# Performance work log

Measured on AMD Instinct MI355X. Metric: run time of the kernel, lower is better.

Reference implementation:

```python
import jax, jax.numpy as jnp
import numpy as np

B, F, V, DW, H, K, T = 32, 2048, 12000, 300, 512, 3, 32
START_ID, END_ID = 1, 2
NEG = -1e9


def lstm(x, h, c, Wx, Wh, b):
    # BasicLSTMCell with forget_bias=1.0
    z = x @ Wx + h @ Wh + b  # [N, 4H]
    i, f, g, o = jnp.split(z, 4, axis=-1)
    c2 = jax.nn.sigmoid(f + 1.0) * c + jax.nn.sigmoid(i) * jnp.tanh(g)
    h2 = jax.nn.sigmoid(o) * jnp.tanh(c2)
    return h2, c2


def beam_decode(E, Wx, Wh, b, Wl, bl, img):
    Bn = img.shape[0]
    img_t = jnp.repeat(img, K, axis=0)  # tile_batch: [B*K, F]
    h = jnp.zeros((Bn * K, H), img.dtype)
    c = jnp.zeros_like(h)
    beam_lp = jnp.tile(jnp.array([0.0] + [NEG] * (K - 1), img.dtype), (Bn, 1))  # [B,K]
    prev = jnp.full((Bn, K), START_ID, jnp.int32)
    finished = jnp.zeros((Bn, K), bool)
    lengths = jnp.zeros((Bn, K), jnp.int32)
    ids = jnp.zeros((Bn, K, T), jnp.int32)
    end_row = jnp.where(jnp.arange(V) == END_ID, 0.0, NEG)  # finished beams only emit END

    def step(carry, t):
        h, c, beam_lp, prev, finished, lengths, ids = carry
        x = jnp.concatenate([E[prev.reshape(-1)], img_t], axis=-1)  # [B*K, DW+F]
        h2, c2 = lstm(x, h, c, Wx, Wh, b)
        lp = jax.nn.log_softmax(h2 @ Wl + bl).reshape(Bn, K, V)
        lp = jnp.where(finished[:, :, None], end_row, lp)
        total = (beam_lp[:, :, None] + lp).reshape(Bn, K * V)
        scores, idx = jax.lax.top_k(total, K)  # [B,K]
        parent = idx // V
        word = (idx % V).astype(jnp.int32)
        g2 = lambda a: jnp.take_along_axis(a, parent, axis=1)
        g3 = lambda a: jnp.take_along_axis(a, parent[:, :, None], axis=1)
        h2 = g3(h2.reshape(Bn, K, H)).reshape(Bn * K, H)
        c2 = g3(c2.reshape(Bn, K, H)).reshape(Bn * K, H)
        ids = g3(ids).at[:, :, t].set(word)  # reorder hypotheses, append word
        fin_p = g2(finished)
        len_p = g2(lengths)
        lengths = jnp.where(fin_p, len_p, len_p + 1)
        finished = fin_p | (word == END_ID)
        return (h2, c2, scores, word, finished, lengths, ids), None

    carry, _ = jax.lax.scan(step, (h, c, beam_lp, prev, finished, lengths, ids), jnp.arange(T))
    return carry[6], carry[5]  # ids [B,K,T], lengths [B,K]


def teacher_rnn(E, Wx, Wh, b, img_t, seq_inputs, lengths):
    # dynamic_rnn semantics: zero outputs and frozen state past sequence_length
    N, L = seq_inputs.shape
    emb = E[seq_inputs]  # [N, L, DW]
    h0 = jnp.zeros((N, H), E.dtype)
    c0 = jnp.zeros_like(h0)

    def step(carry, xs):
        h, c = carry
        x_t, t = xs
        xin = jnp.concatenate([x_t, img_t], axis=-1)
        h2, c2 = lstm(xin, h, c, Wx, Wh, b)
        active = (t < lengths)[:, None]
        h = jnp.where(active, h2, h)
        c = jnp.where(active, c2, c)
        return (h, c), jnp.where(active, h2, 0.0)

    _, outs = jax.lax.scan(step, (h0, c0), (emb.transpose(1, 0, 2), jnp.arange(L)))
    return outs.transpose(1, 0, 2)  # [N, L, H]


def setup_inputs() -> dict:
    key = jax.random.key(0)
    ks = jax.random.split(key, 6)
    return {
        "mean_image_features": jax.random.normal(ks[0], (B, F), jnp.float32),
        "embeddings": jax.random.normal(ks[1], (V, DW), jnp.float32) * 0.1,
        "Wx": jax.random.normal(ks[2], (DW + F, 4 * H), jnp.float32) / np.sqrt(DW + F),
        "Wh": jax.random.normal(ks[3], (H, 4 * H), jnp.float32) / np.sqrt(H),
        "b_lstm": jnp.zeros((4 * H,), jnp.float32),
        "W_logits": jax.random.normal(ks[4], (H, V), jnp.float32) / np.sqrt(H),
        "b_logits": jnp.zeros((V,), jnp.float32),
    }


def reference(mean_image_features, embeddings, Wx, Wh, b_lstm, W_logits, b_logits):
    Bn = mean_image_features.shape[0]
    ids, lengths = beam_decode(embeddings, Wx, Wh, b_lstm, W_logits, b_logits, mean_image_features)
    seq_inputs = jnp.concatenate(
        [jnp.full((Bn, K, 1), START_ID, jnp.int32), ids], axis=2
    ).reshape(Bn * K, T + 1)
    img_t = jnp.repeat(mean_image_features, K, axis=0)
    acts = teacher_rnn(embeddings, Wx, Wh, b_lstm, img_t, seq_inputs, lengths.reshape(-1))
    logits = (acts @ W_logits + b_logits).reshape(Bn, K, T + 1, V)
    return logits, jnp.argmax(logits, axis=-1).astype(jnp.int32)
```

## Files before the change

kernel.cpp:

```cpp
#include <hip/hip_runtime.h>
#include <hip/hip_bf16.h>
#include <math.h>

#define NB   32
#define FDIM 2048
#define VV   12000
#define DWW  300
#define HH   512
#define KW   3
#define TDEC 32
#define SEQ  33
#define NK   96
#define G4   2048
#define START_ID 1
#define END_ID   2
#define NROWS 3168
#define NLB   188
#define INTMX 0x7fffffff
#define FLOORF (-3.0e38f)

typedef float f4v __attribute__((ext_vector_type(4)));
__device__ __forceinline__ void nt_store4(float* p, float4 v){
  f4v t; t.x=v.x; t.y=v.y; t.z=v.z; t.w=v.w;
  __builtin_nontemporal_store(t, (f4v*)p);
}

__device__ __forceinline__ float sigf(float x){ return 1.0f/(1.0f+expf(-x)); }

__device__ __forceinline__ unsigned short f2b(float x){
  __hip_bfloat16 b = __float2bfloat16(x);
  return *reinterpret_cast<unsigned short*>(&b);
}

__device__ __forceinline__ void ins3(float v, int i, float tv[3], int ti[3]){
  if (v > tv[0] || (v == tv[0] && i < ti[0])){
    tv[2]=tv[1]; ti[2]=ti[1]; tv[1]=tv[0]; ti[1]=ti[0]; tv[0]=v; ti[0]=i;
  } else if (v > tv[1] || (v == tv[1] && i < ti[1])){
    tv[2]=tv[1]; ti[2]=ti[1]; tv[1]=v; ti[1]=i;
  } else if (v > tv[2] || (v == tv[2] && i < ti[2])){
    tv[2]=v; ti[2]=i;
  }
}

struct SArgs {
  const float *E, *Wx, *Wh, *Wl, *blog;
  float *P, *c2, *h2s, *zp, *partA, *beam_lp, *rowamax;
  int *prev, *finished, *lengths, *parst, *rowsrc;
  void *Lst;
};

__global__ __launch_bounds__(128) void k_pimg(const float* __restrict__ img,
                                              const float* __restrict__ Wx,
                                              float* __restrict__ parts)
{
  int colb = blockIdx.x, fb = blockIdx.y, tid = threadIdx.x;
  int col = colb*128 + tid;
  int f0 = fb*128;
  __shared__ float s_img[32][128];
  for (int r=0;r<32;r++) s_img[r][tid] = img[r*FDIM + f0 + tid];
  __syncthreads();
  float acc[32];
  #pragma unroll
  for (int r=0;r<32;r++) acc[r]=0.f;
  for (int f2=0; f2<128; ++f2){
    float w = Wx[(size_t)(DWW + f0 + f2)*G4 + col];
    #pragma unroll
    for (int r=0;r<32;r++) acc[r] += w * s_img[r][f2];
  }
  #pragma unroll
  for (int r=0;r<32;r++) parts[(size_t)fb*(32*G4) + r*G4 + col] = acc[r];
}

__global__ __launch_bounds__(512) void k_prep(const float* __restrict__ parts,
    const float* __restrict__ bls, const float* __restrict__ blog,
    float* __restrict__ P, float* __restrict__ beam_lp, int* __restrict__ prev,
    int* __restrict__ finished, int* __restrict__ lengths, float* __restrict__ bamax)
{
  int bid = blockIdx.x, tid = threadIdx.x;
  int gid = bid*512 + tid;
  float s = bls[gid & (G4-1)];
  for (int fb=0; fb<16; ++fb) s += parts[(size_t)fb*(32*G4) + gid];
  P[gid] = s;
  if (bid==0 && tid<NK){
    beam_lp[tid] = (tid%KW==0)?0.f:-1e9f;
    prev[tid]=START_ID; finished[tid]=0; lengths[tid]=0;
  }
  if (bid==2){
    __shared__ float s_rf[8]; __shared__ int s_ri[8];
    float bv=FLOORF; int bi=INTMX;
    for (int i=tid;i<VV;i+=512){
      float v=blog[i];
      if (v>bv || (v==bv && i<bi)){ bv=v; bi=i; }
    }
    #pragma unroll
    for (int d=1;d<64;d<<=1){
      float ov=__shfl_xor(bv,d); int oi=__shfl_xor(bi,d);
      if (ov>bv || (ov==bv && oi<bi)){ bv=ov; bi=oi; }
    }
    if ((tid&63)==0){ s_rf[tid>>6]=bv; s_ri[tid>>6]=bi; }
    __syncthreads();
    if (tid==0){
      for (int w=1;w<8;w++)
        if (s_rf[w]>bv || (s_rf[w]==bv && s_ri[w]<bi)){ bv=s_rf[w]; bi=s_ri[w]; }
      bamax[0] = (float)bi;
    }
  }
}

__global__ __launch_bounds__(512) void k_z(SArgs a, int t)
{
  int bid = blockIdx.x, tid = threadIdx.x;
  __shared__ float smem[96*17 + 16*64];
  __shared__ int sprev[NK], spar[NK];
  if (t>0 && tid<NK){ sprev[tid]=a.prev[tid]; spar[tid]=a.parst[(t-1)*NK+tid]; }
  __syncthreads();

  int colblk = bid & 31, p = bid >> 5;
  int col0 = colblk*64;
  int ks = p*104, ke = ks+104; if (ke>812) ke=812;
  float* sA = smem;
  float* sB = smem + 96*17;
  int tx = tid&15, ty = tid>>4;
  float4 acc[3];
  #pragma unroll
  for (int r=0;r<3;r++) acc[r]=make_float4(0.f,0.f,0.f,0.f);
  for (int k0=ks;k0<ke;k0+=16){
    int bk = ke-k0; if (bk>16) bk=16;
    for (int i=tid;i<96*16;i+=512){
      int n=i>>4, kk=i&15;
      float v=0.f;
      if (kk<bk){
        int kg=k0+kk;
        if (kg<DWW){
          int w = (t==0)?START_ID:sprev[n];
          v = a.E[(size_t)w*DWW+kg];
        } else if (t>0){
          v = a.h2s[((size_t)(t-1)*NK + spar[n])*HH + (kg-DWW)];
        }
      }
      sA[n*17+kk]=v;
    }
    for (int i=tid;i<16*64;i+=512){
      int kk=i>>6, cc=i&63;
      float v=0.f;
      if (kk<bk){
        int kg=k0+kk;
        v = (kg<DWW) ? a.Wx[(size_t)kg*G4+col0+cc] : a.Wh[(size_t)(kg-DWW)*G4+col0+cc];
      }
      sB[i]=v;
    }
    __syncthreads();
    #pragma unroll
    for (int kk=0;kk<16;++kk){
      float4 b4 = *(const float4*)&sB[kk*64+tx*4];
      #pragma unroll
      for (int rr=0;rr<3;rr++){
        float av = sA[(ty+rr*32)*17+kk];
        acc[rr].x += av*b4.x; acc[rr].y += av*b4.y;
        acc[rr].z += av*b4.z; acc[rr].w += av*b4.w;
      }
    }
    __syncthreads();
  }
  float* zpp = a.zp + (size_t)p*NK*G4;
  #pragma unroll
  for (int rr=0;rr<3;rr++)
    *(float4*)&zpp[(size_t)(ty+rr*32)*G4 + col0 + tx*4] = acc[rr];
}

__global__ __launch_bounds__(512) void k_g(SArgs a, int t)
{
  int n = blockIdx.x, m = threadIdx.x;
  int bb = n/KW;
  int par = (t>0) ? a.parst[(t-1)*NK + n] : 0;
  const float* Pr = a.P + (size_t)bb*G4;
  float zi=Pr[m], zf=Pr[HH+m], zg=Pr[2*HH+m], zo=Pr[3*HH+m];
  for (int p=0;p<8;p++){
    const float* zz = a.zp + (size_t)p*NK*G4 + (size_t)n*G4;
    zi+=zz[m]; zf+=zz[HH+m]; zg+=zz[2*HH+m]; zo+=zz[3*HH+m];
  }
  float cold = (t==0) ? 0.f : a.c2[(size_t)((t-1)&1)*NK*HH + (size_t)par*HH + m];
  float c2v = sigf(zf+1.0f)*cold + sigf(zi)*tanhf(zg);
  float h2v = sigf(zo)*tanhf(c2v);
  a.c2[(size_t)(t&1)*NK*HH + (size_t)n*HH + m] = c2v;
  a.h2s[((size_t)t*NK+n)*HH + m] = h2v;
}

template<int BF>
__global__ __launch_bounds__(512) void k_l(SArgs a, int t)
{
  __shared__ float smem[96*36 + 32*64];
  const int bid = blockIdx.x, tid = threadIdx.x;
  const int col0 = bid*64;
  float* sAl = smem;
  float* sBl = smem + 96*36;
  const int tx=tid&15, ty=tid>>4;
  float4 acc[3];
  #pragma unroll
  for (int r=0;r<3;r++) acc[r]=make_float4(0.f,0.f,0.f,0.f);
  for (int k0=0;k0<HH;k0+=32){
    for (int i=tid;i<768;i+=512){
      int row=i>>3, kq=(i&7)*4;
      *(float4*)&sAl[row*36+kq] = *(const float4*)&a.h2s[((size_t)t*NK+row)*HH + k0+kq];
    }
    {
      int kk=tid>>4, c4=(tid&15)*4;
      int col=col0+c4;
      float4 v = make_float4(0.f,0.f,0.f,0.f);
      if (col < VV) v = *(const float4*)&a.Wl[(size_t)(k0+kk)*VV+col];
      *(float4*)&sBl[kk*64+c4]=v;
    }
    __syncthreads();
    #pragma unroll
    for (int kk=0;kk<32;++kk){
      float4 b4 = *(const float4*)&sBl[kk*64+tx*4];
      #pragma unroll
      for (int rr=0;rr<3;rr++){
        float av = sAl[(ty+rr*32)*36+kk];
        acc[rr].x += av*b4.x; acc[rr].y += av*b4.y;
        acc[rr].z += av*b4.z; acc[rr].w += av*b4.w;
      }
    }
    __syncthreads();
  }
  int colg = col0 + tx*4;
  bool cval = colg < VV;
  float4 bias = make_float4(0.f,0.f,0.f,0.f);
  if (cval) bias = *(const float4*)&a.blog[colg];
  #pragma unroll
  for (int rr=0;rr<3;rr++){
    int row = ty + rr*32;
    float v0,v1,v2,v3;
    if (cval){
      v0=acc[rr].x+bias.x; v1=acc[rr].y+bias.y;
      v2=acc[rr].z+bias.z; v3=acc[rr].w+bias.w;
      size_t off = (size_t)(t*NK+row)*VV + colg;
      if (BF){
        ushort4 u;
        u.x=f2b(v0); u.y=f2b(v1); u.z=f2b(v2); u.w=f2b(v3);
        *(ushort4*)((unsigned short*)a.Lst + off) = u;
      } else {
        nt_store4((float*)a.Lst + off, make_float4(v0,v1,v2,v3));
      }
    } else { v0=v1=v2=v3=-INFINITY; }
    float m = fmaxf(fmaxf(v0,v1),fmaxf(v2,v3));
    #pragma unroll
    for (int d=1;d<16;d<<=1) m = fmaxf(m,__shfl_xor(m,d));
    float tv[3]={-INFINITY,-INFINITY,-INFINITY};
    int   ti[3]={INTMX,INTMX,INTMX};
    float s=0.f;
    if (cval){
      ins3(v0,colg,tv,ti); ins3(v1,colg+1,tv,ti);
      ins3(v2,colg+2,tv,ti); ins3(v3,colg+3,tv,ti);
      s = expf(v0-m)+expf(v1-m)+expf(v2-m)+expf(v3-m);
    }
    #pragma unroll
    for (int d=1;d<16;d<<=1){
      s += __shfl_xor(s,d);
      float p0=__shfl_xor(tv[0],d),p1=__shfl_xor(tv[1],d),p2=__shfl_xor(tv[2],d);
      int q0=__shfl_xor(ti[0],d),q1=__shfl_xor(ti[1],d),q2=__shfl_xor(ti[2],d);
      ins3(p0,q0,tv,ti); ins3(p1,q1,tv,ti); ins3(p2,q2,tv,ti);
    }
    if (tx==0){
      float* rp = a.partA + ((size_t)row*NLB + bid)*8;
      *(float4*)rp = make_float4(m,s,tv[0],tv[1]);
      *((float4*)rp+1) = make_float4(tv[2],__int_as_float(ti[0]),__int_as_float(ti[1]),__int_as_float(ti[2]));
    }
  }
}

__global__ __launch_bounds__(512) void k_s(SArgs a, int t)
{
  __shared__ float s_lse[KW], s_tv3[KW*3];
  __shared__ int   s_ti3[KW*3];
  int b = blockIdx.x, tid = threadIdx.x;
  int wv = tid>>6, lane = tid&63;
  if (wv < KW){
    int n = b*KW+wv;
    float M=FLOORF, S=0.f;
    float tv[3]={FLOORF,FLOORF,FLOORF}; int ti[3]={INTMX,INTMX,INTMX};
    for (int i=lane;i<NLB;i+=64){
      const float* rp = a.partA + ((size_t)n*NLB+i)*8;
      float4 r0=*(const float4*)rp, r1=*((const float4*)rp+1);
      float nm = fmaxf(M,r0.x);
      S = S*expf(M-nm) + r0.y*expf(r0.x-nm);
      M = nm;
      ins3(r0.z,__float_as_int(r1.y),tv,ti);
      ins3(r0.w,__float_as_int(r1.z),tv,ti);
      ins3(r1.x,__float_as_int(r1.w),tv,ti);
    }
    #pragma unroll
    for (int d=1;d<64;d<<=1){
      float Mo=__shfl_xor(M,d), So=__shfl_xor(S,d);
      float nm=fmaxf(M,Mo);
      S = S*expf(M-nm)+So*expf(Mo-nm);
      M=nm;
      float p0=__shfl_xor(tv[0],d),p1=__shfl_xor(tv[1],d),p2=__shfl_xor(tv[2],d);
      int q0=__shfl_xor(ti[0],d),q1=__shfl_xor(ti[1],d),q2=__shfl_xor(ti[2],d);
      ins3(p0,q0,tv,ti); ins3(p1,q1,tv,ti); ins3(p2,q2,tv,ti);
    }
    if (lane==0){
      s_lse[wv] = M + logf(S);
      #pragma unroll
      for (int j=0;j<3;j++){ s_tv3[wv*3+j]=tv[j]; s_ti3[wv*3+j]=ti[j]; }
      a.rowamax[t*NK+n] = (float)ti[0];
    }
  }
  __syncthreads();
  if (tid==0){
    float cv[3]={FLOORF,FLOORF,FLOORF}; int cf[3]={INTMX,INTMX,INTMX};
    for (int k=0;k<KW;k++){
      int n=b*KW+k;
      if (a.finished[n]){
        ins3(a.beam_lp[n], k*VV+END_ID, cv,cf);
      } else {
        float blp=a.beam_lp[n], lse=s_lse[k];
        for (int j=0;j<3;j++)
          ins3(blp + (s_tv3[k*3+j]-lse), k*VV+s_ti3[k*3+j], cv,cf);
      }
    }
    int fin_old[KW], len_old[KW];
    for (int j=0;j<KW;j++){ fin_old[j]=a.finished[b*KW+j]; len_old[j]=a.lengths[b*KW+j]; }
    for (int kp=0;kp<KW;kp++){
      int par=cf[kp]/VV, word=cf[kp]-par*VV;
      a.beam_lp[b*KW+kp]=cv[kp];
      a.prev[b*KW+kp]=word;
      a.parst[t*NK + b*KW+kp] = b*KW+par;
      int fp=fin_old[par];
      a.lengths[b*KW+kp] = fp?len_old[par]:(len_old[par]+1);
      a.finished[b*KW+kp] = fp | (word==END_ID);
    }
  }
}

__global__ __launch_bounds__(128) void k_backtrack(const int* __restrict__ parst,
                                                   const int* __restrict__ lengths,
                                                   int* __restrict__ rowsrc)
{
  int n = threadIdx.x;
  if (n >= NK) return;
  int b = n / KW;
  int len = lengths[n];
  rowsrc[n*SEQ + TDEC] = -1;
  int a = n;
  for (int tau = TDEC-1; tau >= 1; --tau){
    int p = parst[tau*NK + a];
    rowsrc[n*SEQ + tau] = (tau < len) ? (tau*NK + p) : -1;
    a = p;
  }
  rowsrc[n*SEQ + 0] = b*KW;
}

template<int BF>
__global__ __launch_bounds__(512) void k_gather(const void* __restrict__ Lst,
    const int* __restrict__ rowsrc, const float* __restrict__ rowamax,
    const float* __restrict__ bamax, const float* __restrict__ blog,
    float* __restrict__ out)
{
  int row = blockIdx.x, tid = threadIdx.x;
  int src = rowsrc[row];
  float* orow = out + (size_t)row*VV;
  if (src >= 0){
    if (BF){
      const unsigned short* L = (const unsigned short*)Lst + (size_t)src*VV;
      for (int j=tid;j<VV/4;j+=512){
        ushort4 u = *(const ushort4*)&L[j*4];
        float4 v;
        v.x = __uint_as_float(((unsigned)u.x)<<16);
        v.y = __uint_as_float(((unsigned)u.y)<<16);
        v.z = __uint_as_float(((unsigned)u.z)<<16);
        v.w = __uint_as_float(((unsigned)u.w)<<16);
        nt_store4(&orow[j*4], v);
      }
    } else {
      const float* L = (const float*)Lst + (size_t)src*VV;
      for (int j=tid;j<VV/4;j+=512){
        float4 v = *(const float4*)&L[j*4];
        nt_store4(&orow[j*4], v);
      }
    }
    if (tid==0) out[(size_t)NROWS*VV + row] = rowamax[src];
  } else {
    for (int j=tid;j<VV/4;j+=512){
      float4 v = *(const float4*)&blog[j*4];
      nt_store4(&orow[j*4], v);
    }
    if (tid==0) out[(size_t)NROWS*VV + row] = bamax[0];
  }
}

extern "C" void kernel_launch(void* const* d_in, const int* in_sizes, int n_in,
                              void* d_out, int out_size, void* d_ws, size_t ws_size,
                              hipStream_t stream) {
  (void)in_sizes; (void)n_in; (void)out_size;
  const float* img  = (const float*)d_in[0];
  const float* E    = (const float*)d_in[1];
  const float* Wx   = (const float*)d_in[2];
  const float* Wh   = (const float*)d_in[3];
  const float* bls  = (const float*)d_in[4];
  const float* Wl   = (const float*)d_in[5];
  const float* blog = (const float*)d_in[6];
  float* out = (float*)d_out;

  float* ws = (float*)d_ws;
  size_t o = 0;
  float* P       = ws+o; o += (size_t)NB*G4;
  float* c2      = ws+o; o += (size_t)2*NK*HH;
  float* h2s     = ws+o; o += (size_t)TDEC*NK*HH;
  float* zp      = ws+o; o += (size_t)8*NK*G4;
  float* partA   = ws+o; o += (size_t)NK*NLB*8;
  float* beam_lp = ws+o; o += 128;
  float* rowamax = ws+o; o += (size_t)TDEC*NK;
  float* bamax   = ws+o; o += 4;
  int* prev      = (int*)(ws+o); o += 128;
  int* finished  = (int*)(ws+o); o += 128;
  int* lengths   = (int*)(ws+o); o += 128;
  int* parst     = (int*)(ws+o); o += (size_t)TDEC*NK;
  int* rowsrc    = (int*)(ws+o); o += 3328;
  o = (o+3) & ~(size_t)3;
  void* Lst      = (void*)(ws+o);

  bool f32 = (ws_size/4 > o) && ((ws_size/4 - o) >= (size_t)TDEC*NK*VV);

  SArgs a;
  a.E=E; a.Wx=Wx; a.Wh=Wh; a.Wl=Wl; a.blog=blog;
  a.P=P; a.c2=c2; a.h2s=h2s; a.zp=zp; a.partA=partA;
  a.beam_lp=beam_lp; a.rowamax=rowamax;
  a.prev=prev; a.finished=finished; a.lengths=lengths; a.parst=parst; a.rowsrc=rowsrc;
  a.Lst=Lst;

  k_pimg<<<dim3(16,16),128,0,stream>>>(img, Wx, zp);
  k_prep<<<128,512,0,stream>>>(zp, bls, blog, P, beam_lp, prev, finished, lengths, bamax);

  if (f32){
    for (int t=0;t<TDEC;t++){
      k_z<<<256,512,0,stream>>>(a,t);
      k_g<<<NK,512,0,stream>>>(a,t);
      k_l<0><<<NLB,512,0,stream>>>(a,t);
      k_s<<<NB,512,0,stream>>>(a,t);
    }
    k_backtrack<<<1,128,0,stream>>>(parst, lengths, rowsrc);
    k_gather<0><<<NROWS,512,0,stream>>>(Lst,rowsrc,rowamax,bamax,blog,out);
  } else {
    for (int t=0;t<TDEC;t++){
      k_z<<<256,512,0,stream>>>(a,t);
      k_g<<<NK,512,0,stream>>>(a,t);
      k_l<1><<<NLB,512,0,stream>>>(a,t);
      k_s<<<NB,512,0,stream>>>(a,t);
    }
    k_backtrack<<<1,128,0,stream>>>(parst, lengths, rowsrc);
    k_gather<1><<<NROWS,512,0,stream>>>(Lst,rowsrc,rowamax,bamax,blog,out);
  }
}
```

Baseline: 2.608 ms.

## Fuse LSTM gate GEMM and cell update into one kernel without split-K

Replaces the split-K gate GEMM (k_z writing 8 partial slabs) and the separate gate/cell kernel (k_g) with a single kernel. Each block owns two hidden units across all four gates, so it computes the full K reduction and applies the LSTM nonlinearities directly. This removes one launch per step and the global round trip of the partial sums. The cost is that each block now runs the full 812-long reduction serially, and its column tile is narrow (8 columns), so reuse of the staged A tile is low and every block reloads all of A.

```diff
diff --git a/kernel.cpp b/kernel.cpp
--- a/kernel.cpp
+++ b/kernel.cpp
@@ -44,7 +44,7 @@
 
 struct SArgs {
   const float *E, *Wx, *Wh, *Wl, *blog;
-  float *P, *c2, *h2s, *zp, *partA, *beam_lp, *rowamax;
+  float *P, *c2, *h2s, *partA, *beam_lp, *rowamax;
   int *prev, *finished, *lengths, *parst, *rowsrc;
   void *Lst;
 };
@@ -107,83 +107,79 @@
   }
 }
 
-__global__ __launch_bounds__(512) void k_z(SArgs a, int t)
-{
-  int bid = blockIdx.x, tid = threadIdx.x;
-  __shared__ float smem[96*17 + 16*64];
+__global__ __launch_bounds__(512) void k_zg(SArgs a, int t)
+{
+  __shared__ float sA[96*65];
+  __shared__ float sB[64*8];
+  __shared__ float zl[96*8];
   __shared__ int sprev[NK], spar[NK];
-  if (t>0 && tid<NK){ sprev[tid]=a.prev[tid]; spar[tid]=a.parst[(t-1)*NK+tid]; }
+  const int j = blockIdx.x, tid = threadIdx.x;
+  if (tid<NK){
+    sprev[tid] = (t==0) ? START_ID : a.prev[tid];
+    spar[tid]  = (t>0) ? a.parst[(t-1)*NK+tid] : 0;
+  }
   __syncthreads();
 
-  int colblk = bid & 31, p = bid >> 5;
-  int col0 = colblk*64;
-  int ks = p*104, ke = ks+104; if (ke>812) ke=812;
-  float* sA = smem;
-  float* sB = smem + 96*17;
-  int tx = tid&15, ty = tid>>4;
-  float4 acc[3];
-  #pragma unroll
-  for (int r=0;r<3;r++) acc[r]=make_float4(0.f,0.f,0.f,0.f);
-  for (int k0=ks;k0<ke;k0+=16){
-    int bk = ke-k0; if (bk>16) bk=16;
-    for (int i=tid;i<96*16;i+=512){
-      int n=i>>4, kk=i&15;
-      float v=0.f;
-      if (kk<bk){
-        int kg=k0+kk;
-        if (kg<DWW){
-          int w = (t==0)?START_ID:sprev[n];
-          v = a.E[(size_t)w*DWW+kg];
+  const int r = tid>>3, c = tid&7;
+  float acc0 = 0.f, acc1 = 0.f;
+
+  for (int k0=0; k0<812; k0+=64){
+    #pragma unroll
+    for (int s=0; s<3; ++s){
+      int idx = tid + s*512;
+      int n = idx>>4, kq = (idx&15)*4;
+      int kg = k0+kq;
+      float4 v = make_float4(0.f,0.f,0.f,0.f);
+      if (kg < 812){
+        if (kg < DWW){
+          v = *(const float4*)&a.E[(size_t)sprev[n]*DWW + kg];
         } else if (t>0){
-          v = a.h2s[((size_t)(t-1)*NK + spar[n])*HH + (kg-DWW)];
+          v = *(const float4*)&a.h2s[((size_t)(t-1)*NK + spar[n])*HH + (kg-DWW)];
         }
       }
-      sA[n*17+kk]=v;
-    }
-    for (int i=tid;i<16*64;i+=512){
-      int kk=i>>6, cc=i&63;
-      float v=0.f;
-      if (kk<bk){
-        int kg=k0+kk;
-        v = (kg<DWW) ? a.Wx[(size_t)kg*G4+col0+cc] : a.Wh[(size_t)(kg-DWW)*G4+col0+cc];
-      }
-      sB[i]=v;
+      sA[n*65+kq  ]=v.x; sA[n*65+kq+1]=v.y;
+      sA[n*65+kq+2]=v.z; sA[n*65+kq+3]=v.w;
+    }
+    if (tid < 256){
+      int kk = tid>>2, q = tid&3;
+      int kg = k0+kk;
+      float2 v = make_float2(0.f,0.f);
+      if (kg < 812){
+        const float* W = (kg<DWW) ? (a.Wx + (size_t)kg*G4 + q*512 + 2*j)
+                                  : (a.Wh + (size_t)(kg-DWW)*G4 + q*512 + 2*j);
+        v = *(const float2*)W;
+      }
+      sB[kk*8 + q*2  ] = v.x;
+      sB[kk*8 + q*2+1] = v.y;
     }
     __syncthreads();
-    #pragma unroll
-    for (int kk=0;kk<16;++kk){
-      float4 b4 = *(const float4*)&sB[kk*64+tx*4];
-      #pragma unroll
-      for (int rr=0;rr<3;rr++){
-        float av = sA[(ty+rr*32)*17+kk];
-        acc[rr].x += av*b4.x; acc[rr].y += av*b4.y;
-        acc[rr].z += av*b4.z; acc[rr].w += av*b4.w;
-      }
+    #pragma unroll 8
+    for (int kk=0; kk<64; ++kk){
+      float bv = sB[kk*8+c];
+      acc0 += sA[r*65+kk] * bv;
+      if (r < 32) acc1 += sA[(r+64)*65+kk] * bv;
     }
     __syncthreads();
   }
-  float* zpp = a.zp + (size_t)p*NK*G4;
-  #pragma unroll
-  for (int rr=0;rr<3;rr++)
-    *(float4*)&zpp[(size_t)(ty+rr*32)*G4 + col0 + tx*4] = acc[rr];
-}
-
-__global__ __launch_bounds__(512) void k_g(SArgs a, int t)
-{
-  int n = blockIdx.x, m = threadIdx.x;
-  int bb = n/KW;
-  int par = (t>0) ? a.parst[(t-1)*NK + n] : 0;
-  const float* Pr = a.P + (size_t)bb*G4;
-  float zi=Pr[m], zf=Pr[HH+m], zg=Pr[2*HH+m], zo=Pr[3*HH+m];
-  for (int p=0;p<8;p++){
-    const float* zz = a.zp + (size_t)p*NK*G4 + (size_t)n*G4;
-    zi+=zz[m]; zf+=zz[HH+m]; zg+=zz[2*HH+m]; zo+=zz[3*HH+m];
-  }
-  float cold = (t==0) ? 0.f : a.c2[(size_t)((t-1)&1)*NK*HH + (size_t)par*HH + m];
-  float c2v = sigf(zf+1.0f)*cold + sigf(zi)*tanhf(zg);
-  float h2v = sigf(zo)*tanhf(c2v);
-  a.c2[(size_t)(t&1)*NK*HH + (size_t)n*HH + m] = c2v;
-  a.h2s[((size_t)t*NK+n)*HH + m] = h2v;
+
+  zl[r*8+c] = acc0;
+  if (r < 32) zl[(r+64)*8+c] = acc1;
+  __syncthreads();
+
+  if (tid < 192){
+    int n = tid>>1, mmbit = tid&1;
+    int m = 2*j + mmbit;
+    const float* Pr = a.P + (size_t)(n/KW)*G4;
+    float zi = zl[n*8+mmbit  ] + Pr[m];
+    float zf = zl[n*8+mmbit+2] + Pr[HH+m];
+    float zg = zl[n*8+mmbit+4] + Pr[2*HH+m];
+    float zo = zl[n*8+mmbit+6] + Pr[3*HH+m];
+    float cold = (t==0) ? 0.f : a.c2[(size_t)((t-1)&1)*NK*HH + (size_t)spar[n]*HH + m];
+    float c2v = sigf(zf+1.0f)*cold + sigf(zi)*tanhf(zg);
+    float h2v = sigf(zo)*tanhf(c2v);
+    a.c2[(size_t)(t&1)*NK*HH + (size_t)n*HH + m] = c2v;
+    a.h2s[((size_t)t*NK+n)*HH + m] = h2v;
+  }
 }
 
 template<int BF>
@@ -407,7 +403,7 @@
   float* P       = ws+o; o += (size_t)NB*G4;
   float* c2      = ws+o; o += (size_t)2*NK*HH;
   float* h2s     = ws+o; o += (size_t)TDEC*NK*HH;
-  float* zp      = ws+o; o += (size_t)8*NK*G4;
+  float* parts   = ws+o; o += (size_t)16*32*G4;
   float* partA   = ws+o; o += (size_t)NK*NLB*8;
   float* beam_lp = ws+o; o += 128;
   float* rowamax = ws+o; o += (size_t)TDEC*NK;
@@ -424,18 +420,17 @@
 
   SArgs a;
   a.E=E; a.Wx=Wx; a.Wh=Wh; a.Wl=Wl; a.blog=blog;
-  a.P=P; a.c2=c2; a.h2s=h2s; a.zp=zp; a.partA=partA;
+  a.P=P; a.c2=c2; a.h2s=h2s; a.partA=partA;
   a.beam_lp=beam_lp; a.rowamax=rowamax;
   a.prev=prev; a.finished=finished; a.lengths=lengths; a.parst=parst; a.rowsrc=rowsrc;
   a.Lst=Lst;
 
-  k_pimg<<<dim3(16,16),128,0,stream>>>(img, Wx, zp);
-  k_prep<<<128,512,0,stream>>>(zp, bls, blog, P, beam_lp, prev, finished, lengths, bamax);
+  k_pimg<<<dim3(16,16),128,0,stream>>>(img, Wx, parts);
+  k_prep<<<128,512,0,stream>>>(parts, bls, blog, P, beam_lp, prev, finished, lengths, bamax);
 
   if (f32){
     for (int t=0;t<TDEC;t++){
-      k_z<<<256,512,0,stream>>>(a,t);
-      k_g<<<NK,512,0,stream>>>(a,t);
+      k_zg<<<256,512,0,stream>>>(a,t);
       k_l<0><<<NLB,512,0,stream>>>(a,t);
       k_s<<<NB,512,0,stream>>>(a,t);
     }
@@ -443,8 +438,7 @@
     k_gather<0><<<NROWS,512,0,stream>>>(Lst,rowsrc,rowamax,bamax,blog,out);
   } else {
     for (int t=0;t<TDEC;t++){
-      k_z<<<256,512,0,stream>>>(a,t);
-      k_g<<<NK,512,0,stream>>>(a,t);
+      k_zg<<<256,512,0,stream>>>(a,t);
       k_l<1><<<NLB,512,0,stream>>>(a,t);
       k_s<<<NB,512,0,stream>>>(a,t);
     }
```

New measurement: 3.892 ms. 49.2% more time.

## Fuse LSTM gate kernel into z-GEMM via last-block atomic counter; fold backtrack into k_s

Applied to the files above, without the earlier changes.

Each k_z block now computes a column slice that covers matching i/f/g/o columns (colblk*16 across the four gates). An atomic per-(t,colblk) counter lets the last of the 8 k-split blocks reduce the partials and apply the LSTM cell update, which removes the separate k_g launch at each of the 32 steps. The backtrack kernel is folded into the final k_s step, and the gather uses nontemporal loads. This saves a launch per step and some round-trips, at the cost of serialized tail work in one block per column group and the overhead of atomic acquire/release.

```diff
diff --git a/kernel.cpp b/kernel.cpp
--- a/kernel.cpp
+++ b/kernel.cpp
@@ -24,6 +24,10 @@
   f4v t; t.x=v.x; t.y=v.y; t.z=v.z; t.w=v.w;
   __builtin_nontemporal_store(t, (f4v*)p);
 }
+__device__ __forceinline__ float4 nt_load4(const float* p){
+  f4v t = __builtin_nontemporal_load((const f4v*)p);
+  return make_float4(t.x,t.y,t.z,t.w);
+}
 
 __device__ __forceinline__ float sigf(float x){ return 1.0f/(1.0f+expf(-x)); }
 
@@ -45,7 +49,7 @@
 struct SArgs {
   const float *E, *Wx, *Wh, *Wl, *blog;
   float *P, *c2, *h2s, *zp, *partA, *beam_lp, *rowamax;
-  int *prev, *finished, *lengths, *parst, *rowsrc;
+  int *prev, *finished, *lengths, *parst, *rowsrc, *gcnt;
   void *Lst;
 };
 
@@ -74,13 +78,15 @@
 __global__ __launch_bounds__(512) void k_prep(const float* __restrict__ parts,
     const float* __restrict__ bls, const float* __restrict__ blog,
     float* __restrict__ P, float* __restrict__ beam_lp, int* __restrict__ prev,
-    int* __restrict__ finished, int* __restrict__ lengths, float* __restrict__ bamax)
+    int* __restrict__ finished, int* __restrict__ lengths, int* __restrict__ gcnt,
+    float* __restrict__ bamax)
 {
   int bid = blockIdx.x, tid = threadIdx.x;
   int gid = bid*512 + tid;
   float s = bls[gid & (G4-1)];
   for (int fb=0; fb<16; ++fb) s += parts[(size_t)fb*(32*G4) + gid];
   P[gid] = s;
+  if (gid < TDEC*32) gcnt[gid] = 0;
   if (bid==0 && tid<NK){
     beam_lp[tid] = (tid%KW==0)?0.f:-1e9f;
     prev[tid]=START_ID; finished[tid]=0; lengths[tid]=0;
@@ -107,16 +113,16 @@
   }
 }
 
-__global__ __launch_bounds__(512) void k_z(SArgs a, int t)
+__global__ __launch_bounds__(512) void k_zg(SArgs a, int t)
 {
   int bid = blockIdx.x, tid = threadIdx.x;
   __shared__ float smem[96*17 + 16*64];
   __shared__ int sprev[NK], spar[NK];
+  __shared__ int s_old;
   if (t>0 && tid<NK){ sprev[tid]=a.prev[tid]; spar[tid]=a.parst[(t-1)*NK+tid]; }
   __syncthreads();
 
   int colblk = bid & 31, p = bid >> 5;
-  int col0 = colblk*64;
   int ks = p*104, ke = ks+104; if (ke>812) ke=812;
   float* sA = smem;
   float* sB = smem + 96*17;
@@ -145,7 +151,8 @@
       float v=0.f;
       if (kk<bk){
         int kg=k0+kk;
-        v = (kg<DWW) ? a.Wx[(size_t)kg*G4+col0+cc] : a.Wh[(size_t)(kg-DWW)*G4+col0+cc];
+        int colg = colblk*16 + (cc&15) + (cc>>4)*512;
+        v = (kg<DWW) ? a.Wx[(size_t)kg*G4+colg] : a.Wh[(size_t)(kg-DWW)*G4+colg];
       }
       sB[i]=v;
     }
@@ -162,28 +169,35 @@
     }
     __syncthreads();
   }
-  float* zpp = a.zp + (size_t)p*NK*G4;
-  #pragma unroll
-  for (int rr=0;rr<3;rr++)
-    *(float4*)&zpp[(size_t)(ty+rr*32)*G4 + col0 + tx*4] = acc[rr];
-}
-
-__global__ __launch_bounds__(512) void k_g(SArgs a, int t)
-{
-  int n = blockIdx.x, m = threadIdx.x;
-  int bb = n/KW;
-  int par = (t>0) ? a.parst[(t-1)*NK + n] : 0;
-  const float* Pr = a.P + (size_t)bb*G4;
-  float zi=Pr[m], zf=Pr[HH+m], zg=Pr[2*HH+m], zo=Pr[3*HH+m];
-  for (int p=0;p<8;p++){
-    const float* zz = a.zp + (size_t)p*NK*G4 + (size_t)n*G4;
-    zi+=zz[m]; zf+=zz[HH+m]; zg+=zz[2*HH+m]; zo+=zz[3*HH+m];
-  }
-  float cold = (t==0) ? 0.f : a.c2[(size_t)((t-1)&1)*NK*HH + (size_t)par*HH + m];
-  float c2v = sigf(zf+1.0f)*cold + sigf(zi)*tanhf(zg);
-  float h2v = sigf(zo)*tanhf(c2v);
-  a.c2[(size_t)(t&1)*NK*HH + (size_t)n*HH + m] = c2v;
-  a.h2s[((size_t)t*NK+n)*HH + m] = h2v;
+  {
+    float* zpp = a.zp + (size_t)p*NK*G4;
+    int cc4 = tx*4;
+    int colg = colblk*16 + (cc4&15) + (cc4>>4)*512;
+    #pragma unroll
+    for (int rr=0;rr<3;rr++)
+      *(float4*)&zpp[(size_t)(ty+rr*32)*G4 + colg] = acc[rr];
+  }
+  __syncthreads();
+  if (tid==0)
+    s_old = __hip_atomic_fetch_add(&a.gcnt[t*32+colblk], 1, __ATOMIC_ACQ_REL, __HIP_MEMORY_SCOPE_AGENT);
+  __syncthreads();
+  if (s_old != 7) return;
+
+  for (int oi=tid; oi<NK*16; oi+=512){
+    int n=oi>>4, mm=oi&15;
+    int m = colblk*16+mm;
+    const float* Pr = a.P + (size_t)(n/KW)*G4;
+    float zi=Pr[m], zf=Pr[HH+m], zg=Pr[2*HH+m], zo=Pr[3*HH+m];
+    for (int pp=0;pp<8;pp++){
+      const float* zz = a.zp + (size_t)pp*NK*G4 + (size_t)n*G4;
+      zi+=zz[m]; zf+=zz[HH+m]; zg+=zz[2*HH+m]; zo+=zz[3*HH+m];
+    }
+    float cold = (t==0) ? 0.f : a.c2[(size_t)((t-1)&1)*NK*HH + (size_t)spar[n]*HH + m];
+    float c2v = sigf(zf+1.0f)*cold + sigf(zi)*tanhf(zg);
+    float h2v = sigf(zo)*tanhf(c2v);
+    a.c2[(size_t)(t&1)*NK*HH + (size_t)n*HH + m] = c2v;
+    a.h2s[((size_t)t*NK+n)*HH + m] = h2v;
+  }
 }
 
 template<int BF>
@@ -331,24 +345,21 @@
       a.finished[b*KW+kp] = fp | (word==END_ID);
     }
   }
-}
-
-__global__ __launch_bounds__(128) void k_backtrack(const int* __restrict__ parst,
-                                                   const int* __restrict__ lengths,
-                                                   int* __restrict__ rowsrc)
-{
-  int n = threadIdx.x;
-  if (n >= NK) return;
-  int b = n / KW;
-  int len = lengths[n];
-  rowsrc[n*SEQ + TDEC] = -1;
-  int a = n;
-  for (int tau = TDEC-1; tau >= 1; --tau){
-    int p = parst[tau*NK + a];
-    rowsrc[n*SEQ + tau] = (tau < len) ? (tau*NK + p) : -1;
-    a = p;
-  }
-  rowsrc[n*SEQ + 0] = b*KW;
+  if (t == TDEC-1){
+    __syncthreads();
+    if (tid < KW){
+      int n = b*KW + tid;
+      int len = a.lengths[n];
+      a.rowsrc[n*SEQ+TDEC] = -1;
+      int cur = n;
+      for (int tau=TDEC-1; tau>=1; --tau){
+        int p = a.parst[tau*NK+cur];
+        a.rowsrc[n*SEQ+tau] = (tau<len) ? (tau*NK+p) : -1;
+        cur = p;
+      }
+      a.rowsrc[n*SEQ+0] = b*KW;
+    }
+  }
 }
 
 template<int BF>
@@ -375,7 +386,7 @@
     } else {
       const float* L = (const float*)Lst + (size_t)src*VV;
       for (int j=tid;j<VV/4;j+=512){
-        float4 v = *(const float4*)&L[j*4];
+        float4 v = nt_load4(&L[j*4]);
         nt_store4(&orow[j*4], v);
       }
     }
@@ -417,6 +428,7 @@
   int* lengths   = (int*)(ws+o); o += 128;
   int* parst     = (int*)(ws+o); o += (size_t)TDEC*NK;
   int* rowsrc    = (int*)(ws+o); o += 3328;
+  int* gcnt      = (int*)(ws+o); o += (size_t)TDEC*32;
   o = (o+3) & ~(size_t)3;
   void* Lst      = (void*)(ws+o);
 
@@ -427,28 +439,25 @@
   a.P=P; a.c2=c2; a.h2s=h2s; a.zp=zp; a.partA=partA;
   a.beam_lp=beam_lp; a.rowamax=rowamax;
   a.prev=prev; a.finished=finished; a.lengths=lengths; a.parst=parst; a.rowsrc=rowsrc;
+  a.gcnt=gcnt;
   a.Lst=Lst;
 
   k_pimg<<<dim3(16,16),128,0,stream>>>(img, Wx, zp);
-  k_prep<<<128,512,0,stream>>>(zp, bls, blog, P, beam_lp, prev, finished, lengths, bamax);
+  k_prep<<<128,512,0,stream>>>(zp, bls, blog, P, beam_lp, prev, finished, lengths, gcnt, bamax);
 
   if (f32){
     for (int t=0;t<TDEC;t++){
-      k_z<<<256,512,0,stream>>>(a,t);
-      k_g<<<NK,512,0,stream>>>(a,t);
+      k_zg<<<256,512,0,stream>>>(a,t);
       k_l<0><<<NLB,512,0,stream>>>(a,t);
       k_s<<<NB,512,0,stream>>>(a,t);
     }
-    k_backtrack<<<1,128,0,stream>>>(parst, lengths, rowsrc);
     k_gather<0><<<NROWS,512,0,stream>>>(Lst,rowsrc,rowamax,bamax,blog,out);
   } else {
     for (int t=0;t<TDEC;t++){
-      k_z<<<256,512,0,stream>>>(a,t);
-      k_g<<<NK,512,0,stream>>>(a,t);
+      k_zg<<<256,512,0,stream>>>(a,t);
       k_l<1><<<NLB,512,0,stream>>>(a,t);
       k_s<<<NB,512,0,stream>>>(a,t);
     }
-    k_backtrack<<<1,128,0,stream>>>(parst, lengths, rowsrc);
     k_gather<1><<<NROWS,512,0,stream>>>(Lst,rowsrc,rowamax,bamax,blog,out);
   }
 }
```

Result: slower. 3.008 ms (+15.3%).
